# Kernel tuning notes

Hardware: AMD Instinct MI355X
Metric: run time of the kernel (lower is better)

The kernel has to match this reference:

```python
import jax, jax.numpy as jnp
import numpy as np

DIM = 1024
N_HEADS = 16
HEAD_DIM = DIM // N_HEADS
EPS = 1e-05
ROPE_BASE = 1000000.0


def apply_rope(x, base=ROPE_BASE):
    # x: [b, seq, heads, head_dim]
    b, seq, n_heads, dim = x.shape
    half = dim // 2
    i = jnp.arange(half)
    theta = 1.0 / base ** (2 * i / dim)
    pos = jnp.arange(seq)
    angles = pos[:, None] * theta[None, :]            # [seq, half]
    cos = jnp.cos(angles)[None, :, None, :]           # [1, seq, 1, half]
    sin = jnp.sin(angles)[None, :, None, :]
    x1, x2 = jnp.split(x, 2, axis=-1)
    return jnp.concatenate([x1 * cos - x2 * sin, x1 * sin + x2 * cos], axis=-1)


def setup_inputs() -> dict:
    key = jax.random.key(0)
    ks = jax.random.split(key, 6)
    b, seq = 2, 2048
    scale = 1.0 / np.sqrt(DIM)
    x = jax.random.normal(ks[0], (b, seq, DIM), dtype=jnp.float32)
    w_norm = jnp.ones((DIM,), dtype=jnp.float32)
    Wq = jax.random.normal(ks[1], (DIM, DIM), dtype=jnp.float32) * scale
    Wk = jax.random.normal(ks[2], (DIM, DIM), dtype=jnp.float32) * scale
    Wv = jax.random.normal(ks[3], (DIM, DIM), dtype=jnp.float32) * scale
    Wo = jax.random.normal(ks[4], (DIM, DIM), dtype=jnp.float32) * scale
    return {"x": x, "w_norm": w_norm, "Wq": Wq, "Wk": Wk, "Wv": Wv, "Wo": Wo}


def reference(x, w_norm, Wq, Wk, Wv, Wo):
    b, seq, d = x.shape
    # RMSNorm
    rms = jnp.sqrt(jnp.mean(x * x, axis=-1, keepdims=True) + EPS)
    x_norm = x / rms * w_norm
    # QKV projections (Dense without bias: y = x @ W)
    q = (x_norm @ Wq).reshape(b, seq, N_HEADS, HEAD_DIM)
    k = (x_norm @ Wk).reshape(b, seq, N_HEADS, HEAD_DIM)
    v = (x_norm @ Wv).reshape(b, seq, N_HEADS, HEAD_DIM)
    q = apply_rope(q)
    k = apply_rope(k)
    # Causal attention with full [b,h,t,s] scores (faithful to source)
    scores = jnp.einsum('bthd,bshd->bhts', q, k) / jnp.sqrt(jnp.float32(HEAD_DIM))
    causal = jnp.triu(jnp.full((seq, seq), -jnp.inf, dtype=scores.dtype), k=1)
    scores = scores + causal[None, None, :, :]
    attn = jax.nn.softmax(scores, axis=-1)
    out = jnp.einsum('bhts,bshd->bthd', attn, v).reshape(b, seq, d)
    return out @ Wo
```

## Files before the change

### kernel.cpp

```cpp
#include <hip/hip_runtime.h>

#define DIM 1024
#define SEQ 2048
#define BATCH 2
#define NHEADS 16
#define HD 64
#define ROWS (BATCH * SEQ)

typedef __bf16 bf16x8 __attribute__((ext_vector_type(8)));
typedef __bf16 bf16x4 __attribute__((ext_vector_type(4)));
typedef float f32x4 __attribute__((ext_vector_type(4)));
typedef float f32x16 __attribute__((ext_vector_type(16)));
typedef unsigned u32x4 __attribute__((ext_vector_type(4)));

__device__ __forceinline__ f32x4 f4zero() {
    f32x4 z = {0.f, 0.f, 0.f, 0.f};
    return z;
}

__device__ __forceinline__ unsigned cvtpk(float lo, float hi) {
    unsigned r;
    asm("v_cvt_pk_bf16_f32 %0, %1, %2" : "=v"(r) : "v"(lo), "v"(hi));
    return r;
}

__device__ __forceinline__ void pl32swap(unsigned& a, unsigned& b) {
    asm volatile("v_permlane32_swap_b32 %0, %1" : "+v"(a), "+v"(b));
}

__device__ __forceinline__ int slot_base(int qb) {
    if (qb < 8) return qb;
    if (qb < 16) return 8 + 2 * (qb - 8);
    if (qb < 24) return 24 + 3 * (qb - 16);
    return 48 + 4 * (qb - 24);
}

#define GLOAD_LDS16(g, l)                                                                  \
    __builtin_amdgcn_global_load_lds((const __attribute__((address_space(1))) void*)(g),   \
                                     (__attribute__((address_space(3))) void*)(l), 16, 0, 0)

__global__ __launch_bounds__(256) void rmsnorm_bf16(const float* __restrict__ x,
                                                    const float* __restrict__ w,
                                                    __bf16* __restrict__ xn) {
    int row = blockIdx.x;
    int t = threadIdx.x;
    float4 v = ((const float4*)(x + (size_t)row * DIM))[t];
    float ss = v.x * v.x + v.y * v.y + v.z * v.z + v.w * v.w;
#pragma unroll
    for (int off = 1; off < 64; off <<= 1) ss += __shfl_xor(ss, off);
    __shared__ float red[4];
    if ((t & 63) == 0) red[t >> 6] = ss;
    __syncthreads();
    ss = red[0] + red[1] + red[2] + red[3];
    float scale = rsqrtf(ss * (1.0f / DIM) + 1e-5f);
    float4 wv = ((const float4*)w)[t];
    bf16x4 o;
    o[0] = (__bf16)(v.x * scale * wv.x);
    o[1] = (__bf16)(v.y * scale * wv.y);
    o[2] = (__bf16)(v.z * scale * wv.z);
    o[3] = (__bf16)(v.w * scale * wv.w);
    *(bf16x4*)(xn + (size_t)row * DIM + t * 4) = o;
}

__global__ __launch_bounds__(256) void wcvt_kernel(const float* __restrict__ Wq,
                                                   const float* __restrict__ Wk,
                                                   const float* __restrict__ Wv,
                                                   const float* __restrict__ Wo,
                                                   __bf16* tq, __bf16* tk, __bf16* tv, __bf16* to_) {
    int z = blockIdx.z;
    const float* W = z == 0 ? Wq : z == 1 ? Wk : z == 2 ? Wv : Wo;
    __bf16* T = z == 0 ? tq : z == 1 ? tk : z == 2 ? tv : to_;
    __shared__ float tile[32][33];
    int n0 = blockIdx.x * 32, k0 = blockIdx.y * 32;
    int tx = threadIdx.x & 31, ty = threadIdx.x >> 5;
#pragma unroll
    for (int j = 0; j < 32; j += 8) tile[ty + j][tx] = W[(size_t)(k0 + ty + j) * DIM + n0 + tx];
    __syncthreads();
#pragma unroll
    for (int j = 0; j < 32; j += 8)
        T[(size_t)(n0 + ty + j) * DIM + k0 + tx] = (__bf16)tile[tx][ty + j];
}

__global__ __launch_bounds__(256) void rope_table_kernel(float* __restrict__ cosT,
                                                         float* __restrict__ sinT) {
    int idx = blockIdx.x * 256 + threadIdx.x;
    int s = idx >> 5, i = idx & 31;
    float e = (2.0f * (float)i) / 64.0f;
    float theta = 1.0f / powf(1000000.0f, e);
    float ang = (float)s * theta;
    cosT[idx] = cosf(ang);
    sinT[idx] = sinf(ang);
}

__device__ __forceinline__ void gemm_core(const __bf16* __restrict__ A,
                                          const __bf16* __restrict__ Bt,
                                          int K, __bf16* As, __bf16* Bs,
                                          f32x4 (&acc)[4][4], int row0, int col0) {
    int tid = threadIdx.x;
    int w = tid >> 6, l = tid & 63, l15 = l & 15, g = l >> 4;
    int wr = (w >> 1) << 6, wc = (w & 1) << 6;

    int sr0 = tid >> 2;
    int sr1 = 64 + (tid >> 2);
    int lc0 = (((tid & 3) ^ ((tid >> 3) & 3)) << 3);
    const __bf16* gA0 = A + (size_t)(row0 + sr0) * K + lc0;
    const __bf16* gA1 = A + (size_t)(row0 + sr1) * K + lc0;
    const __bf16* gB0 = Bt + (size_t)(col0 + sr0) * K + lc0;
    const __bf16* gB1 = Bt + (size_t)(col0 + sr1) * K + lc0;
    __bf16* lA0 = As + w * 512;
    __bf16* lA1 = As + 2048 + w * 512;
    __bf16* lB0 = Bs + w * 512;
    __bf16* lB1 = Bs + 2048 + w * 512;

    int rca = ((g ^ ((l15 >> 1) & 3)) << 3);

#pragma unroll
    for (int i = 0; i < 4; ++i)
#pragma unroll
        for (int j = 0; j < 4; ++j) acc[i][j] = f4zero();

    for (int k0 = 0; k0 < K; k0 += 32) {
        __syncthreads();
        GLOAD_LDS16(gA0 + k0, lA0);
        GLOAD_LDS16(gA1 + k0, lA1);
        GLOAD_LDS16(gB0 + k0, lB0);
        GLOAD_LDS16(gB1 + k0, lB1);
        __syncthreads();

        bf16x8 af[4], bfr[4];
#pragma unroll
        for (int i = 0; i < 4; ++i) af[i] = *(const bf16x8*)&As[(wr + i * 16 + l15) * 32 + rca];
#pragma unroll
        for (int j = 0; j < 4; ++j) bfr[j] = *(const bf16x8*)&Bs[(wc + j * 16 + l15) * 32 + rca];
        __builtin_amdgcn_s_setprio(1);
#pragma unroll
        for (int i = 0; i < 4; ++i)
#pragma unroll
            for (int j = 0; j < 4; ++j)
                acc[i][j] = __builtin_amdgcn_mfma_f32_16x16x32_bf16(af[i], bfr[j], acc[i][j], 0, 0, 0);
        __builtin_amdgcn_s_setprio(0);
    }
}

__global__ __launch_bounds__(256) void gemm_qkv_kernel(const __bf16* __restrict__ xn,
                                                       const __bf16* __restrict__ wq,
                                                       const __bf16* __restrict__ wk,
                                                       const __bf16* __restrict__ wv,
                                                       __bf16* __restrict__ qo,
                                                       __bf16* __restrict__ ko,
                                                       __bf16* __restrict__ vt,
                                                       const float* __restrict__ cosT,
                                                       const float* __restrict__ sinT) {
    __shared__ __bf16 As[128 * 32];
    __shared__ __bf16 Bs[128 * 32];
    int bid = blockIdx.x;
    int tid = threadIdx.x;
    int w = tid >> 6, l = tid & 63, l15 = l & 15, g = l >> 4;
    int wr = (w >> 1) << 6, wc = (w & 1) << 6;
    f32x4 acc[4][4];

    if (bid < 512) {
        int z = bid >> 8, t = bid & 255;
        int col0 = (t & 7) << 7, row0 = (t >> 3) << 7;
        gemm_core(xn, z ? wk : wq, DIM, As, Bs, acc, row0, col0);
        __bf16* C = z ? ko : qo;
        int colbase = col0 + wc;
#pragma unroll
        for (int i = 0; i < 4; ++i) {
#pragma unroll
            for (int r = 0; r < 4; ++r) {
                int row = row0 + wr + i * 16 + g * 4 + r;
                int s = row & (SEQ - 1);
#pragma unroll
                for (int j = 0; j < 2; ++j) {
                    float c = cosT[s * 32 + j * 16 + l15];
                    float sn = sinT[s * 32 + j * 16 + l15];
                    float x1 = acc[i][j][r], x2 = acc[i][j + 2][r];
                    C[(size_t)row * DIM + colbase + j * 16 + l15] = (__bf16)(x1 * c - x2 * sn);
                    C[(size_t)row * DIM + colbase + (j + 2) * 16 + l15] = (__bf16)(x1 * sn + x2 * c);
                }
            }
        }
    } else {
        int t = bid - 512;
        int b = t >> 7, r7 = t & 127;
        int row0 = (r7 >> 4) << 7;
        int col0 = (r7 & 15) << 7;
        gemm_core(wv, xn + (size_t)b * SEQ * DIM, DIM, As, Bs, acc, row0, col0);
        __bf16* C = vt + (size_t)b * (NHEADS * HD) * SEQ;
#pragma unroll
        for (int i = 0; i < 4; ++i)
#pragma unroll
            for (int j = 0; j < 4; ++j)
#pragma unroll
                for (int r = 0; r < 4; ++r) {
                    int row = row0 + wr + i * 16 + g * 4 + r;
                    int col = col0 + wc + j * 16 + l15;
                    C[(size_t)row * SEQ + col] = (__bf16)acc[i][j][r];
                }
    }
}

__global__ __launch_bounds__(256) void gemm_out_kernel(const __bf16* __restrict__ ctx,
                                                       const __bf16* __restrict__ wo,
                                                       float* __restrict__ out) {
    __shared__ __bf16 As[128 * 32];
    __shared__ __bf16 Bs[128 * 32];
    int row0 = (int)blockIdx.y << 7, col0 = (int)blockIdx.x << 7;
    f32x4 acc[4][4];
    gemm_core(ctx, wo, DIM, As, Bs, acc, row0, col0);
    int tid = threadIdx.x;
    int w = tid >> 6, l = tid & 63, l15 = l & 15, g = l >> 4;
    int wr = (w >> 1) << 6, wc = (w & 1) << 6;
#pragma unroll
    for (int i = 0; i < 4; ++i)
#pragma unroll
        for (int j = 0; j < 4; ++j)
#pragma unroll
            for (int r = 0; r < 4; ++r) {
                int row = row0 + wr + i * 16 + g * 4 + r;
                int col = col0 + wc + j * 16 + l15;
                out[(size_t)row * DIM + col] = acc[i][j][r];
            }
}

__global__ __launch_bounds__(128) void attn_mfma_kernel(const __bf16* __restrict__ q,
                                                        const __bf16* __restrict__ k,
                                                        const __bf16* __restrict__ vt,
                                                        __bf16* __restrict__ part_O,
                                                        float* __restrict__ part_ml) {
    int bh = blockIdx.x;
    int slot = 79 - (int)blockIdx.y;
    int qb, ci;
    if (slot < 8) { qb = slot; ci = 0; }
    else if (slot < 24) { int t = slot - 8; qb = 8 + (t >> 1); ci = t & 1; }
    else if (slot < 48) { int t = slot - 24; qb = 16 + t / 3; ci = t - 3 * (qb - 16); }
    else { int t = slot - 48; qb = 24 + (t >> 2); ci = t & 3; }
    int nch = (qb >> 3) + 1;
    int ntiles = (ci == nch - 1) ? (qb + 1 - (ci << 3)) : 8;
    int ks0 = ci << 9;

    int b = bh >> 4, h = bh & 15;
    __shared__ __bf16 Ks[64][72];
    __shared__ __bf16 Vs[64][72];
    int tid = threadIdx.x, w = tid >> 6, l = tid & 63;
    int l31 = l & 31, hi = l >> 5;
    size_t hoff = (size_t)(b * SEQ) * DIM + h * HD;
    const __bf16* vth = vt + (size_t)bh * HD * SEQ;
    int qw0 = qb * 64 + w * 32;
    int qrow = qw0 + l31;

    bf16x8 qf[4];
    const float c2 = 0.125f * 1.44269504f;
#pragma unroll
    for (int g = 0; g < 4; ++g) {
        bf16x8 t0 = *(const bf16x8*)&q[hoff + (size_t)qrow * DIM + g * 16 + hi * 8];
#pragma unroll
        for (int e = 0; e < 8; ++e) qf[g][e] = (__bf16)((float)t0[e] * c2);
    }

    f32x16 oA, oB;
#pragma unroll
    for (int r = 0; r < 16; ++r) {
        oA[r] = 0.f;
        oB[r] = 0.f;
    }
    float m_run = -1e30f, l_run = 0.f;

    int sr = tid >> 3, sc = (tid & 7) * 8;
    bf16x8 rk[4], rv[4];
#pragma unroll
    for (int c = 0; c < 4; ++c) {
        rk[c] = *(const bf16x8*)&k[hoff + (size_t)(ks0 + c * 16 + sr) * DIM + sc];
        rv[c] = *(const bf16x8*)&vth[(size_t)(c * 16 + sr) * SEQ + ks0 + sc];
    }

    for (int st = 0; st < ntiles; ++st) {
        int s0 = ks0 + (st << 6);
        __syncthreads();
#pragma unroll
        for (int c = 0; c < 4; ++c) {
            *(bf16x8*)&Ks[c * 16 + sr][sc] = rk[c];
            *(bf16x8*)&Vs[c * 16 + sr][sc] = rv[c];
        }
        __syncthreads();
        if (st + 1 < ntiles) {
            int sn = s0 + 64;
#pragma unroll
            for (int c = 0; c < 4; ++c) {
                rk[c] = *(const bf16x8*)&k[hoff + (size_t)(sn + c * 16 + sr) * DIM + sc];
                rv[c] = *(const bf16x8*)&vth[(size_t)(c * 16 + sr) * SEQ + sn + sc];
            }
        }

        f32x16 sa, sb;
#pragma unroll
        for (int r = 0; r < 16; ++r) {
            sa[r] = 0.f;
            sb[r] = 0.f;
        }
        __builtin_amdgcn_s_setprio(1);
#pragma unroll
        for (int g = 0; g < 4; ++g) {
            bf16x8 ka = *(const bf16x8*)&Ks[l31][g * 16 + hi * 8];
            bf16x8 kb2 = *(const bf16x8*)&Ks[32 + l31][g * 16 + hi * 8];
            sa = __builtin_amdgcn_mfma_f32_32x32x16_bf16(ka, qf[g], sa, 0, 0, 0);
            sb = __builtin_amdgcn_mfma_f32_32x32x16_bf16(kb2, qf[g], sb, 0, 0, 0);
        }
        __builtin_amdgcn_s_setprio(0);

        if (s0 + 63 > qw0) {
#pragma unroll
            for (int r = 0; r < 16; ++r) {
                int kg = s0 + (r & 3) + 8 * (r >> 2) + 4 * hi;
                if (kg > qrow) sa[r] = -1e30f;
                if (kg + 32 > qrow) sb[r] = -1e30f;
            }
        }

        float lmax = -3e38f;
#pragma unroll
        for (int r = 0; r < 16; ++r) lmax = fmaxf(lmax, fmaxf(sa[r], sb[r]));
        if (!__all(lmax <= m_run + 10.0f)) {
            float omax = fmaxf(lmax, __shfl_xor(lmax, 32));
            float m_new = fmaxf(m_run, omax);
            float alpha = exp2f(m_run - m_new);
            l_run *= alpha;
#pragma unroll
            for (int r = 0; r < 16; ++r) {
                oA[r] *= alpha;
                oB[r] *= alpha;
            }
            m_run = m_new;
        }
        float ls = 0.f;
#pragma unroll
        for (int r = 0; r < 16; ++r) {
            sa[r] = exp2f(sa[r] - m_run);
            ls += sa[r];
            sb[r] = exp2f(sb[r] - m_run);
            ls += sb[r];
        }
        l_run += ls + __shfl_xor(ls, 32);

        bf16x8 pa[4];
#pragma unroll
        for (int g = 0; g < 2; ++g) {
            unsigned a_ = cvtpk(sa[8 * g + 0], sa[8 * g + 1]);
            unsigned b_ = cvtpk(sa[8 * g + 4], sa[8 * g + 5]);
            pl32swap(a_, b_);
            unsigned c_ = cvtpk(sa[8 * g + 2], sa[8 * g + 3]);
            unsigned d_ = cvtpk(sa[8 * g + 6], sa[8 * g + 7]);
            pl32swap(c_, d_);
            u32x4 t4 = {a_, c_, b_, d_};
            pa[g] = __builtin_bit_cast(bf16x8, t4);
        }
#pragma unroll
        for (int g = 0; g < 2; ++g) {
            unsigned a_ = cvtpk(sb[8 * g + 0], sb[8 * g + 1]);
            unsigned b_ = cvtpk(sb[8 * g + 4], sb[8 * g + 5]);
            pl32swap(a_, b_);
            unsigned c_ = cvtpk(sb[8 * g + 2], sb[8 * g + 3]);
            unsigned d_ = cvtpk(sb[8 * g + 6], sb[8 * g + 7]);
            pl32swap(c_, d_);
            u32x4 t4 = {a_, c_, b_, d_};
            pa[2 + g] = __builtin_bit_cast(bf16x8, t4);
        }

        __builtin_amdgcn_s_setprio(1);
#pragma unroll
        for (int ks = 0; ks < 4; ++ks) {
            bf16x8 va = *(const bf16x8*)&Vs[l31][ks * 16 + hi * 8];
            bf16x8 vb2 = *(const bf16x8*)&Vs[32 + l31][ks * 16 + hi * 8];
            oA = __builtin_amdgcn_mfma_f32_32x32x16_bf16(va, pa[ks], oA, 0, 0, 0);
            oB = __builtin_amdgcn_mfma_f32_32x32x16_bf16(vb2, pa[ks], oB, 0, 0, 0);
        }
        __builtin_amdgcn_s_setprio(0);
    }

    int gslot = bh * 80 + slot;
    int qloc = w * 32 + l31;
    __bf16* po = part_O + (size_t)gslot * 4096 + qloc * 64;
#pragma unroll
    for (int rr = 0; rr < 16; rr += 4) {
        int d0 = 8 * (rr >> 2) + 4 * hi;
        uint2 pA = {cvtpk(oA[rr], oA[rr + 1]), cvtpk(oA[rr + 2], oA[rr + 3])};
        uint2 pB = {cvtpk(oB[rr], oB[rr + 1]), cvtpk(oB[rr + 2], oB[rr + 3])};
        *(uint2*)&po[d0] = pA;
        *(uint2*)&po[32 + d0] = pB;
    }
    if (hi == 0) {
        part_ml[(size_t)gslot * 128 + qloc] = m_run;
        part_ml[(size_t)gslot * 128 + 64 + qloc] = l_run;
    }
}

__global__ __launch_bounds__(256) void attn_combine_kernel(const __bf16* __restrict__ part_O,
                                                           const float* __restrict__ part_ml,
                                                           __bf16* __restrict__ ctx) {
    int bh = blockIdx.x, qb = blockIdx.y;
    int b = bh >> 4, h = bh & 15;
    int nch = (qb >> 3) + 1;
    int base = slot_base(qb);
    size_t so = (size_t)bh * 80 + base;
    int t = threadIdx.x;
    int row = t >> 2, dseg = (t & 3) << 4;

    float mv0 = -1e30f, mv1 = -1e30f, mv2 = -1e30f, mv3 = -1e30f;
    mv0 = part_ml[(so + 0) * 128 + row];
    if (nch > 1) mv1 = part_ml[(so + 1) * 128 + row];
    if (nch > 2) mv2 = part_ml[(so + 2) * 128 + row];
    if (nch > 3) mv3 = part_ml[(so + 3) * 128 + row];
    float mmax = fmaxf(fmaxf(mv0, mv1), fmaxf(mv2, mv3));

    float acc[16];
#pragma unroll
    for (int e = 0; e < 16; ++e) acc[e] = 0.f;
    float lsum = 0.f;

#pragma unroll 4
    for (int i = 0; i < 4; ++i) {
        if (i >= nch) break;
        float mi = i == 0 ? mv0 : i == 1 ? mv1 : i == 2 ? mv2 : mv3;
        float wsc = exp2f(mi - mmax);
        lsum += wsc * part_ml[(so + i) * 128 + 64 + row];
        const __bf16* po = part_O + (so + i) * 4096 + row * 64 + dseg;
        bf16x8 a = *(const bf16x8*)po;
        bf16x8 b2 = *(const bf16x8*)(po + 8);
#pragma unroll
        for (int e = 0; e < 8; ++e) {
            acc[e] += wsc * (float)a[e];
            acc[8 + e] += wsc * (float)b2[e];
        }
    }

    float inv = 1.0f / lsum;
    bf16x8 oa, ob;
#pragma unroll
    for (int e = 0; e < 8; ++e) {
        oa[e] = (__bf16)(acc[e] * inv);
        ob[e] = (__bf16)(acc[8 + e] * inv);
    }
    size_t off = ((size_t)(b * SEQ) + qb * 64 + row) * DIM + h * HD + dseg;
    *(bf16x8*)&ctx[off] = oa;
    *(bf16x8*)&ctx[off + 8] = ob;
}

extern "C" void kernel_launch(void* const* d_in, const int* in_sizes, int n_in,
                              void* d_out, int out_size, void* d_ws, size_t ws_size,
                              hipStream_t stream) {
    const float* x = (const float*)d_in[0];
    const float* w_norm = (const float*)d_in[1];
    const float* Wq = (const float*)d_in[2];
    const float* Wk = (const float*)d_in[3];
    const float* Wv = (const float*)d_in[4];
    const float* Wo = (const float*)d_in[5];
    float* out = (float*)d_out;
    char* w8 = (char*)d_ws;

    const size_t MB = 1ull << 20;
    __bf16* xn = (__bf16*)(w8);
    __bf16* wtq = (__bf16*)(w8 + 8 * MB);
    __bf16* wtk = (__bf16*)(w8 + 10 * MB);
    __bf16* wtv = (__bf16*)(w8 + 12 * MB);
    __bf16* part_O = (__bf16*)(w8);
    __bf16* wto = (__bf16*)(w8 + 20 * MB);
    __bf16* qb = (__bf16*)(w8 + 22 * MB);
    __bf16* kb = (__bf16*)(w8 + 30 * MB);
    __bf16* vtb = (__bf16*)(w8 + 38 * MB);
    __bf16* ctx = (__bf16*)(w8 + 46 * MB);
    float* cosT = (float*)(w8 + 54 * MB);
    float* sinT = cosT + SEQ * 32;
    float* part_ml = (float*)(w8 + 55 * MB);

    wcvt_kernel<<<dim3(32, 32, 4), 256, 0, stream>>>(Wq, Wk, Wv, Wo, wtq, wtk, wtv, wto);
    rmsnorm_bf16<<<ROWS, 256, 0, stream>>>(x, w_norm, xn);
    rope_table_kernel<<<(SEQ * 32) / 256, 256, 0, stream>>>(cosT, sinT);

    gemm_qkv_kernel<<<768, 256, 0, stream>>>(xn, wtq, wtk, wtv, qb, kb, vtb, cosT, sinT);

    attn_mfma_kernel<<<dim3(BATCH * NHEADS, 80), 128, 0, stream>>>(qb, kb, vtb, part_O, part_ml);
    attn_combine_kernel<<<dim3(BATCH * NHEADS, SEQ / 64), 256, 0, stream>>>(part_O, part_ml, ctx);

    gemm_out_kernel<<<dim3(DIM / 128, ROWS / 128), 256, 0, stream>>>(ctx, wto, out);
}
```

Baseline: 134.2 us.

## Restructure attention into single-wave blocks loading K/V directly from global memory

The attention kernel now runs one 64-thread wave per block over 32 query rows and 32-key tiles, with twice as many split slots. The shared-memory staging and both __syncthreads per tile are removed; each lane loads its K and V MFMA fragments straight from global memory, with K double-buffered in registers. The combine kernel and partial-buffer layout are changed to match the 32-row granularity. This drops block-level synchronization and causal waste at the diagonal, at the cost of losing K/V reuse across waves, which raises global/L2 traffic, and of doubling the partial-result writes.

```diff
diff --git a/kernel.cpp b/kernel.cpp
--- a/kernel.cpp
+++ b/kernel.cpp
@@ -28,11 +28,11 @@
     asm volatile("v_permlane32_swap_b32 %0, %1" : "+v"(a), "+v"(b));
 }
 
-__device__ __forceinline__ int slot_base(int qb) {
-    if (qb < 8) return qb;
-    if (qb < 16) return 8 + 2 * (qb - 8);
-    if (qb < 24) return 24 + 3 * (qb - 16);
-    return 48 + 4 * (qb - 24);
+__device__ __forceinline__ int slot_base(int qp) {
+    if (qp < 16) return qp;
+    if (qp < 32) return 16 + 2 * (qp - 16);
+    if (qp < 48) return 48 + 3 * (qp - 32);
+    return 96 + 4 * (qp - 48);
 }
 
 #define GLOAD_LDS16(g, l)                                                                  \
@@ -224,39 +224,40 @@
             }
 }
 
-__global__ __launch_bounds__(128) void attn_mfma_kernel(const __bf16* __restrict__ q,
-                                                        const __bf16* __restrict__ k,
-                                                        const __bf16* __restrict__ vt,
-                                                        __bf16* __restrict__ part_O,
-                                                        float* __restrict__ part_ml) {
+__global__ __launch_bounds__(64, 3) void attn_mfma_kernel(const __bf16* __restrict__ q,
+                                                          const __bf16* __restrict__ k,
+                                                          const __bf16* __restrict__ vt,
+                                                          __bf16* __restrict__ part_O,
+                                                          float* __restrict__ part_ml) {
     int bh = blockIdx.x;
-    int slot = 79 - (int)blockIdx.y;
-    int qb, ci;
-    if (slot < 8) { qb = slot; ci = 0; }
-    else if (slot < 24) { int t = slot - 8; qb = 8 + (t >> 1); ci = t & 1; }
-    else if (slot < 48) { int t = slot - 24; qb = 16 + t / 3; ci = t - 3 * (qb - 16); }
-    else { int t = slot - 48; qb = 24 + (t >> 2); ci = t & 3; }
-    int nch = (qb >> 3) + 1;
-    int ntiles = (ci == nch - 1) ? (qb + 1 - (ci << 3)) : 8;
+    int slot = 159 - (int)blockIdx.y;
+    int qp, ci;
+    if (slot < 16) { qp = slot; ci = 0; }
+    else if (slot < 48) { int t = slot - 16; qp = 16 + (t >> 1); ci = t & 1; }
+    else if (slot < 96) { int t = slot - 48; qp = 32 + t / 3; ci = t - 3 * (t / 3); }
+    else { int t = slot - 96; qp = 48 + (t >> 2); ci = t & 3; }
+    int local = qp - (ci << 4);
+    int ntiles = local < 16 ? local + 1 : 16;
+    int dtile = local < 16 ? local : -1;
     int ks0 = ci << 9;
 
     int b = bh >> 4, h = bh & 15;
-    __shared__ __bf16 Ks[64][72];
-    __shared__ __bf16 Vs[64][72];
-    int tid = threadIdx.x, w = tid >> 6, l = tid & 63;
+    int l = threadIdx.x & 63;
     int l31 = l & 31, hi = l >> 5;
     size_t hoff = (size_t)(b * SEQ) * DIM + h * HD;
     const __bf16* vth = vt + (size_t)bh * HD * SEQ;
-    int qw0 = qb * 64 + w * 32;
-    int qrow = qw0 + l31;
+    int qrow = qp * 32 + l31;
 
     bf16x8 qf[4];
-    const float c2 = 0.125f * 1.44269504f;
-#pragma unroll
-    for (int g = 0; g < 4; ++g) {
-        bf16x8 t0 = *(const bf16x8*)&q[hoff + (size_t)qrow * DIM + g * 16 + hi * 8];
-#pragma unroll
-        for (int e = 0; e < 8; ++e) qf[g][e] = (__bf16)((float)t0[e] * c2);
+    {
+        const __bf16* qptr = q + hoff + (size_t)qrow * DIM + hi * 8;
+        const float c2 = 0.125f * 1.44269504f;
+#pragma unroll
+        for (int g = 0; g < 4; ++g) {
+            bf16x8 t0 = *(const bf16x8*)(qptr + g * 16);
+#pragma unroll
+            for (int e = 0; e < 8; ++e) qf[g][e] = (__bf16)((float)t0[e] * c2);
+        }
     }
 
     f32x16 oA, oB;
@@ -267,60 +268,49 @@
     }
     float m_run = -1e30f, l_run = 0.f;
 
-    int sr = tid >> 3, sc = (tid & 7) * 8;
-    bf16x8 rk[4], rv[4];
-#pragma unroll
-    for (int c = 0; c < 4; ++c) {
-        rk[c] = *(const bf16x8*)&k[hoff + (size_t)(ks0 + c * 16 + sr) * DIM + sc];
-        rv[c] = *(const bf16x8*)&vth[(size_t)(c * 16 + sr) * SEQ + ks0 + sc];
-    }
-
-    for (int st = 0; st < ntiles; ++st) {
-        int s0 = ks0 + (st << 6);
-        __syncthreads();
-#pragma unroll
-        for (int c = 0; c < 4; ++c) {
-            *(bf16x8*)&Ks[c * 16 + sr][sc] = rk[c];
-            *(bf16x8*)&Vs[c * 16 + sr][sc] = rv[c];
-        }
-        __syncthreads();
+    const __bf16* kptr = k + hoff + (size_t)(ks0 + l31) * DIM + hi * 8;
+    const __bf16* vptr0 = vth + (size_t)l31 * SEQ + ks0 + hi * 8;
+    const __bf16* vptr1 = vth + (size_t)(32 + l31) * SEQ + ks0 + hi * 8;
+
+    bf16x8 ka[4], kb[4];
+#pragma unroll
+    for (int g = 0; g < 4; ++g) ka[g] = *(const bf16x8*)(kptr + g * 16);
+    kptr += 32 * DIM;
+
+    auto tile_body = [&](bf16x8 (&kcur)[4], bf16x8 (&knxt)[4], int st) {
         if (st + 1 < ntiles) {
-            int sn = s0 + 64;
-#pragma unroll
-            for (int c = 0; c < 4; ++c) {
-                rk[c] = *(const bf16x8*)&k[hoff + (size_t)(sn + c * 16 + sr) * DIM + sc];
-                rv[c] = *(const bf16x8*)&vth[(size_t)(c * 16 + sr) * SEQ + sn + sc];
-            }
-        }
-
-        f32x16 sa, sb;
-#pragma unroll
-        for (int r = 0; r < 16; ++r) {
-            sa[r] = 0.f;
-            sb[r] = 0.f;
-        }
+#pragma unroll
+            for (int g = 0; g < 4; ++g) knxt[g] = *(const bf16x8*)(kptr + g * 16);
+            kptr += 32 * DIM;
+        }
+        bf16x8 vv0 = *(const bf16x8*)(vptr0);
+        bf16x8 vv1 = *(const bf16x8*)(vptr0 + 16);
+        bf16x8 vv2 = *(const bf16x8*)(vptr1);
+        bf16x8 vv3 = *(const bf16x8*)(vptr1 + 16);
+        vptr0 += 32;
+        vptr1 += 32;
+
+        f32x16 sa;
+#pragma unroll
+        for (int r = 0; r < 16; ++r) sa[r] = 0.f;
         __builtin_amdgcn_s_setprio(1);
 #pragma unroll
-        for (int g = 0; g < 4; ++g) {
-            bf16x8 ka = *(const bf16x8*)&Ks[l31][g * 16 + hi * 8];
-            bf16x8 kb2 = *(const bf16x8*)&Ks[32 + l31][g * 16 + hi * 8];
-            sa = __builtin_amdgcn_mfma_f32_32x32x16_bf16(ka, qf[g], sa, 0, 0, 0);
-            sb = __builtin_amdgcn_mfma_f32_32x32x16_bf16(kb2, qf[g], sb, 0, 0, 0);
-        }
+        for (int g = 0; g < 4; ++g)
+            sa = __builtin_amdgcn_mfma_f32_32x32x16_bf16(kcur[g], qf[g], sa, 0, 0, 0);
         __builtin_amdgcn_s_setprio(0);
 
-        if (s0 + 63 > qw0) {
+        if (st == dtile) {
+            int s0 = ks0 + (st << 5);
 #pragma unroll
             for (int r = 0; r < 16; ++r) {
                 int kg = s0 + (r & 3) + 8 * (r >> 2) + 4 * hi;
                 if (kg > qrow) sa[r] = -1e30f;
-                if (kg + 32 > qrow) sb[r] = -1e30f;
             }
         }
 
-        float lmax = -3e38f;
-#pragma unroll
-        for (int r = 0; r < 16; ++r) lmax = fmaxf(lmax, fmaxf(sa[r], sb[r]));
+        float lmax = sa[0];
+#pragma unroll
+        for (int r = 1; r < 16; ++r) lmax = fmaxf(lmax, sa[r]);
         if (!__all(lmax <= m_run + 10.0f)) {
             float omax = fmaxf(lmax, __shfl_xor(lmax, 32));
             float m_new = fmaxf(m_run, omax);
@@ -338,49 +328,41 @@
         for (int r = 0; r < 16; ++r) {
             sa[r] = exp2f(sa[r] - m_run);
             ls += sa[r];
-            sb[r] = exp2f(sb[r] - m_run);
-            ls += sb[r];
         }
         l_run += ls + __shfl_xor(ls, 32);
 
-        bf16x8 pa[4];
-#pragma unroll
-        for (int g = 0; g < 2; ++g) {
-            unsigned a_ = cvtpk(sa[8 * g + 0], sa[8 * g + 1]);
-            unsigned b_ = cvtpk(sa[8 * g + 4], sa[8 * g + 5]);
-            pl32swap(a_, b_);
-            unsigned c_ = cvtpk(sa[8 * g + 2], sa[8 * g + 3]);
-            unsigned d_ = cvtpk(sa[8 * g + 6], sa[8 * g + 7]);
-            pl32swap(c_, d_);
-            u32x4 t4 = {a_, c_, b_, d_};
-            pa[g] = __builtin_bit_cast(bf16x8, t4);
-        }
-#pragma unroll
-        for (int g = 0; g < 2; ++g) {
-            unsigned a_ = cvtpk(sb[8 * g + 0], sb[8 * g + 1]);
-            unsigned b_ = cvtpk(sb[8 * g + 4], sb[8 * g + 5]);
-            pl32swap(a_, b_);
-            unsigned c_ = cvtpk(sb[8 * g + 2], sb[8 * g + 3]);
-            unsigned d_ = cvtpk(sb[8 * g + 6], sb[8 * g + 7]);
-            pl32swap(c_, d_);
-            u32x4 t4 = {a_, c_, b_, d_};
-            pa[2 + g] = __builtin_bit_cast(bf16x8, t4);
-        }
+        unsigned a0 = cvtpk(sa[0], sa[1]), b0 = cvtpk(sa[4], sa[5]);
+        pl32swap(a0, b0);
+        unsigned c0 = cvtpk(sa[2], sa[3]), d0 = cvtpk(sa[6], sa[7]);
+        pl32swap(c0, d0);
+        u32x4 t0 = {a0, c0, b0, d0};
+        bf16x8 pa0 = __builtin_bit_cast(bf16x8, t0);
+        unsigned a1 = cvtpk(sa[8], sa[9]), b1 = cvtpk(sa[12], sa[13]);
+        pl32swap(a1, b1);
+        unsigned c1 = cvtpk(sa[10], sa[11]), d1 = cvtpk(sa[14], sa[15]);
+        pl32swap(c1, d1);
+        u32x4 t1 = {a1, c1, b1, d1};
+        bf16x8 pa1 = __builtin_bit_cast(bf16x8, t1);
 
         __builtin_amdgcn_s_setprio(1);
-#pragma unroll
-        for (int ks = 0; ks < 4; ++ks) {
-            bf16x8 va = *(const bf16x8*)&Vs[l31][ks * 16 + hi * 8];
-            bf16x8 vb2 = *(const bf16x8*)&Vs[32 + l31][ks * 16 + hi * 8];
-            oA = __builtin_amdgcn_mfma_f32_32x32x16_bf16(va, pa[ks], oA, 0, 0, 0);
-            oB = __builtin_amdgcn_mfma_f32_32x32x16_bf16(vb2, pa[ks], oB, 0, 0, 0);
-        }
+        oA = __builtin_amdgcn_mfma_f32_32x32x16_bf16(vv0, pa0, oA, 0, 0, 0);
+        oA = __builtin_amdgcn_mfma_f32_32x32x16_bf16(vv1, pa1, oA, 0, 0, 0);
+        oB = __builtin_amdgcn_mfma_f32_32x32x16_bf16(vv2, pa0, oB, 0, 0, 0);
+        oB = __builtin_amdgcn_mfma_f32_32x32x16_bf16(vv3, pa1, oB, 0, 0, 0);
         __builtin_amdgcn_s_setprio(0);
-    }
-
-    int gslot = bh * 80 + slot;
-    int qloc = w * 32 + l31;
-    __bf16* po = part_O + (size_t)gslot * 4096 + qloc * 64;
+    };
+
+    int st = 0;
+    while (st < ntiles) {
+        tile_body(ka, kb, st);
+        ++st;
+        if (st >= ntiles) break;
+        tile_body(kb, ka, st);
+        ++st;
+    }
+
+    int gslot = bh * 160 + slot;
+    __bf16* po = part_O + (size_t)gslot * 2048 + l31 * 64;
 #pragma unroll
     for (int rr = 0; rr < 16; rr += 4) {
         int d0 = 8 * (rr >> 2) + 4 * hi;
@@ -390,27 +372,27 @@
         *(uint2*)&po[32 + d0] = pB;
     }
     if (hi == 0) {
-        part_ml[(size_t)gslot * 128 + qloc] = m_run;
-        part_ml[(size_t)gslot * 128 + 64 + qloc] = l_run;
-    }
-}
-
-__global__ __launch_bounds__(256) void attn_combine_kernel(const __bf16* __restrict__ part_O,
+        part_ml[(size_t)gslot * 64 + l31] = m_run;
+        part_ml[(size_t)gslot * 64 + 32 + l31] = l_run;
+    }
+}
+
+__global__ __launch_bounds__(128) void attn_combine_kernel(const __bf16* __restrict__ part_O,
                                                            const float* __restrict__ part_ml,
                                                            __bf16* __restrict__ ctx) {
-    int bh = blockIdx.x, qb = blockIdx.y;
+    int bh = blockIdx.x, qp = blockIdx.y;
     int b = bh >> 4, h = bh & 15;
-    int nch = (qb >> 3) + 1;
-    int base = slot_base(qb);
-    size_t so = (size_t)bh * 80 + base;
+    int nch = (qp >> 4) + 1;
+    int base = slot_base(qp);
+    size_t so = (size_t)bh * 160 + base;
     int t = threadIdx.x;
     int row = t >> 2, dseg = (t & 3) << 4;
 
     float mv0 = -1e30f, mv1 = -1e30f, mv2 = -1e30f, mv3 = -1e30f;
-    mv0 = part_ml[(so + 0) * 128 + row];
-    if (nch > 1) mv1 = part_ml[(so + 1) * 128 + row];
-    if (nch > 2) mv2 = part_ml[(so + 2) * 128 + row];
-    if (nch > 3) mv3 = part_ml[(so + 3) * 128 + row];
+    mv0 = part_ml[(so + 0) * 64 + row];
+    if (nch > 1) mv1 = part_ml[(so + 1) * 64 + row];
+    if (nch > 2) mv2 = part_ml[(so + 2) * 64 + row];
+    if (nch > 3) mv3 = part_ml[(so + 3) * 64 + row];
     float mmax = fmaxf(fmaxf(mv0, mv1), fmaxf(mv2, mv3));
 
     float acc[16];
@@ -423,8 +405,8 @@
         if (i >= nch) break;
         float mi = i == 0 ? mv0 : i == 1 ? mv1 : i == 2 ? mv2 : mv3;
         float wsc = exp2f(mi - mmax);
-        lsum += wsc * part_ml[(so + i) * 128 + 64 + row];
-        const __bf16* po = part_O + (so + i) * 4096 + row * 64 + dseg;
+        lsum += wsc * part_ml[(so + i) * 64 + 32 + row];
+        const __bf16* po = part_O + (so + i) * 2048 + row * 64 + dseg;
         bf16x8 a = *(const bf16x8*)po;
         bf16x8 b2 = *(const bf16x8*)(po + 8);
 #pragma unroll
@@ -441,7 +423,7 @@
         oa[e] = (__bf16)(acc[e] * inv);
         ob[e] = (__bf16)(acc[8 + e] * inv);
     }
-    size_t off = ((size_t)(b * SEQ) + qb * 64 + row) * DIM + h * HD + dseg;
+    size_t off = ((size_t)(b * SEQ) + qp * 32 + row) * DIM + h * HD + dseg;
     *(bf16x8*)&ctx[off] = oa;
     *(bf16x8*)&ctx[off + 8] = ob;
 }
@@ -479,8 +461,8 @@
 
     gemm_qkv_kernel<<<768, 256, 0, stream>>>(xn, wtq, wtk, wtv, qb, kb, vtb, cosT, sinT);
 
-    attn_mfma_kernel<<<dim3(BATCH * NHEADS, 80), 128, 0, stream>>>(qb, kb, vtb, part_O, part_ml);
-    attn_combine_kernel<<<dim3(BATCH * NHEADS, SEQ / 64), 256, 0, stream>>>(part_O, part_ml, ctx);
+    attn_mfma_kernel<<<dim3(BATCH * NHEADS, 160), 64, 0, stream>>>(qb, kb, vtb, part_O, part_ml);
+    attn_combine_kernel<<<dim3(BATCH * NHEADS, SEQ / 32), 128, 0, stream>>>(part_O, part_ml, ctx);
 
     gemm_out_kernel<<<dim3(DIM / 128, ROWS / 128), 256, 0, stream>>>(ctx, wto, out);
 }
```

New measurement: 159.5 us. +18.9%, slower.
